# Kernel optimization log

Hardware: AMD Instinct MI355X
Metric: run time of the kernel (lower is better)

The kernel has to match this reference:

```python
import jax, jax.numpy as jnp
import numpy as np

B, S, D_MODEL, N_HEADS, HEAD_DIM = 4, 2048, 1024, 16, 64
NEG = -1e9


def apply_rope_real(x, cos_f, sin_f):
    # x: [B, H, S, D]; cos_f/sin_f: [S, D//2] broadcast over B, H
    x_even = x[..., ::2]
    x_odd = x[..., 1::2]
    out_even = x_even * cos_f - x_odd * sin_f
    out_odd = x_even * sin_f + x_odd * cos_f
    return jnp.stack([out_even, out_odd], axis=-1).reshape(x.shape)


def setup_inputs() -> dict:
    key = jax.random.key(0)
    ks = jax.random.split(key, 8)
    x = jax.random.normal(ks[0], (B, S, D_MODEL), dtype=jnp.float32)
    # RoPE tables: theta_i = 10000^{-2i/d}, angles = pos * theta
    inv_freq = 1.0 / (10000.0 ** (jnp.arange(0, HEAD_DIM, 2, dtype=jnp.float32) / HEAD_DIM))
    angles = jnp.arange(S, dtype=jnp.float32)[:, None] * inv_freq[None, :]  # [S, D/2]
    cos_freqs = jnp.cos(angles)
    sin_freqs = jnp.sin(angles)
    causal_mask = jnp.where(jnp.tril(jnp.ones((S, S), dtype=bool)), 0.0, NEG).astype(jnp.float32)
    scale = 0.02
    w_q = jax.random.normal(ks[1], (D_MODEL, D_MODEL), dtype=jnp.float32) * scale
    w_k = jax.random.normal(ks[2], (D_MODEL, D_MODEL), dtype=jnp.float32) * scale
    w_v = jax.random.normal(ks[3], (D_MODEL, D_MODEL), dtype=jnp.float32) * scale
    w_o = jax.random.normal(ks[4], (D_MODEL, D_MODEL), dtype=jnp.float32) * scale
    return {"x": x, "cos_freqs": cos_freqs, "sin_freqs": sin_freqs,
            "causal_mask": causal_mask, "w_q": w_q, "w_k": w_k, "w_v": w_v, "w_o": w_o}


def reference(x, cos_freqs, sin_freqs, causal_mask, w_q, w_k, w_v, w_o):
    batch, seq_len, _ = x.shape
    scale = 1.0 / jnp.sqrt(jnp.float32(HEAD_DIM))
    # torch Linear: y = x @ W.T
    def proj(w):
        return (x @ w.T).reshape(batch, seq_len, N_HEADS, HEAD_DIM).transpose(0, 2, 1, 3)
    q = apply_rope_real(proj(w_q), cos_freqs, sin_freqs)
    k = apply_rope_real(proj(w_k), cos_freqs, sin_freqs)
    v = proj(w_v)
    attn = jnp.einsum('bhqd,bhkd->bhqk', q, k) * scale + causal_mask
    attn = jax.nn.softmax(attn, axis=-1)
    out = jnp.einsum('bhqk,bhkd->bhqd', attn, v)
    out = out.transpose(0, 2, 1, 3).reshape(batch, seq_len, -1)
    return out @ w_o.T
```

## Files before the change

kernel.cpp:

```cpp
#include <hip/hip_runtime.h>
#include <stdint.h>

#define B_  4
#define S_  2048
#define DM_ 1024
#define NH_ 16
#define HD_ 64

typedef unsigned short ushort_t;
typedef __bf16 bf16x8 __attribute__((ext_vector_type(8)));
typedef float  floatx4 __attribute__((ext_vector_type(4)));
typedef float  floatx16 __attribute__((ext_vector_type(16)));

__device__ __forceinline__ float bf2f(ushort_t u) {
    union { unsigned int i; float f; } v; v.i = ((unsigned int)u) << 16; return v.f;
}
__device__ __forceinline__ ushort_t f2bf(float f) {
    union { float f; unsigned int i; } v; v.f = f;
    unsigned int x = v.i;
    return (ushort_t)((x + 0x7fffu + ((x >> 16) & 1u)) >> 16);
}
__device__ __forceinline__ unsigned int pack_bf16_trunc(float lo, float hi) {
    union { float f; unsigned int u; } a, b;
    a.f = lo; b.f = hi;
    return __builtin_amdgcn_perm(b.u, a.u, 0x07060302u);
}

#define QSCALE 0.1803368801f

__global__ __launch_bounds__(256) void cvt_all_kernel(
    const float* __restrict__ x,  const float* __restrict__ wq,
    const float* __restrict__ wk, const float* __restrict__ wv,
    const float* __restrict__ wo,
    ushort_t* __restrict__ xb,  ushort_t* __restrict__ wqb,
    ushort_t* __restrict__ wkb, ushort_t* __restrict__ wvb,
    ushort_t* __restrict__ wob)
{
    const int blk = blockIdx.x;
    const float* src; ushort_t* dst; int off;
    if (blk < 8192)       { src = x;  dst = xb;  off = blk; }
    else if (blk < 9216)  { src = wq; dst = wqb; off = blk - 8192; }
    else if (blk < 10240) { src = wk; dst = wkb; off = blk - 9216; }
    else if (blk < 11264) { src = wv; dst = wvb; off = blk - 10240; }
    else                  { src = wo; dst = wob; off = blk - 11264; }
    const int i = off * 256 + threadIdx.x;
    float4 v = ((const float4*)src)[i];
    ushort4 o; o.x = f2bf(v.x); o.y = f2bf(v.y); o.z = f2bf(v.z); o.w = f2bf(v.w);
    ((ushort4*)dst)[i] = o;
}

__global__ __launch_bounds__(512, 2) void gemm_qkv_kernel(
    const ushort_t* __restrict__ A,
    const ushort_t* __restrict__ B0, const ushort_t* __restrict__ B1,
    const ushort_t* __restrict__ B2,
    void* __restrict__ C0, void* __restrict__ C1, void* __restrict__ C2,
    const float* __restrict__ cf, const float* __restrict__ sf,
    int M, int N, int K, int nz)
{
    __shared__ ushort_t As[2][16384];
    __shared__ ushort_t Bs[2][8192];

    const int lid = blockIdx.x;
    const int cpx = gridDim.x >> 3;
    const int wg  = (lid & 7) * cpx + (lid >> 3);
    const int x   = wg / (8 * nz);
    const int rr  = wg - x * (8 * nz);
    const int y   = rr & 7;
    const int z   = rr >> 3;

    const ushort_t* Bw = z == 0 ? B0 : z == 1 ? B1 : B2;
    void* Cv           = z == 0 ? C0 : z == 1 ? C1 : C2;

    const int tid  = threadIdx.x;
    const int wave = tid >> 6, lane = tid & 63;
    const int l15 = lane & 15, quad = lane >> 4;
    const int wr = wave >> 1, wc = wave & 1;
    const int mbase = x * 256;
    const int nbase = y * 128;
    const int NT = K >> 6;

    auto stageA = [&](int bt, int t, int L0) {
#pragma unroll
        for (int L = L0; L < L0 + 2; ++L) {
            const int e8  = L * 512 + tid;
            const int row = e8 >> 3, c = e8 & 7;
            const ushort_t* src = A + (size_t)(mbase + row) * K + t * 64 + ((c ^ (row & 7)) << 3);
            __builtin_amdgcn_global_load_lds(
                (const __attribute__((address_space(1))) unsigned int*)src,
                (__attribute__((address_space(3))) unsigned int*)(&As[bt][e8 * 8]), 16, 0, 0);
        }
    };
    auto stageB = [&](int bt, int t, int L) {
        const int e8  = L * 512 + tid;
        const int row = e8 >> 3, c = e8 & 7;
        const ushort_t* src = Bw + (size_t)(nbase + row) * K + t * 64 + ((c ^ (row & 7)) << 3);
        __builtin_amdgcn_global_load_lds(
            (const __attribute__((address_space(1))) unsigned int*)src,
            (__attribute__((address_space(3))) unsigned int*)(&Bs[bt][e8 * 8]), 16, 0, 0);
    };

    floatx4 acc[4][4] = {};

    stageA(0, 0, 0); stageA(0, 0, 2);
    stageB(0, 0, 0); stageB(0, 0, 1);
    if (NT > 1) {
        stageB(1, 1, 0); stageB(1, 1, 1);
        asm volatile("s_waitcnt vmcnt(2)" ::: "memory");
    } else {
        asm volatile("s_waitcnt vmcnt(0)" ::: "memory");
    }
    __builtin_amdgcn_s_barrier();

    auto do_tile = [&](int t, int bt) {
        bf16x8 a0[2][2], a1[2][2], b0[2][2], b1[2][2];
#pragma unroll
        for (int kk = 0; kk < 2; ++kk) {
#pragma unroll
            for (int f = 0; f < 2; ++f) {
                const int row = wr * 64 + f * 16 + l15;
                a0[kk][f] = *(const bf16x8*)&As[bt][row * 64 + ((((kk << 2) | quad)) ^ (l15 & 7)) * 8];
            }
#pragma unroll
            for (int g = 0; g < 2; ++g) {
                const int row = wc * 64 + g * 16 + l15;
                b0[kk][g] = *(const bf16x8*)&Bs[bt][row * 64 + ((((kk << 2) | quad)) ^ (l15 & 7)) * 8];
            }
        }
        if (t + 1 < NT) stageA(bt ^ 1, t + 1, 0);
        __builtin_amdgcn_s_barrier();
        asm volatile("s_waitcnt lgkmcnt(0)" ::: "memory");
        __builtin_amdgcn_s_setprio(1);
#pragma unroll
        for (int kk = 0; kk < 2; ++kk)
#pragma unroll
            for (int mt = 0; mt < 2; ++mt)
#pragma unroll
                for (int nt = 0; nt < 2; ++nt)
                    acc[mt][nt] = __builtin_amdgcn_mfma_f32_16x16x32_bf16(
                        a0[kk][mt], b0[kk][nt], acc[mt][nt], 0, 0, 0);
        __builtin_amdgcn_s_setprio(0);
        __builtin_amdgcn_s_barrier();

#pragma unroll
        for (int kk = 0; kk < 2; ++kk)
#pragma unroll
            for (int g = 0; g < 2; ++g) {
                const int row = wc * 64 + 32 + g * 16 + l15;
                b1[kk][g] = *(const bf16x8*)&Bs[bt][row * 64 + ((((kk << 2) | quad)) ^ (l15 & 7)) * 8];
            }
        if (t + 1 < NT) stageA(bt ^ 1, t + 1, 2);
        __builtin_amdgcn_s_barrier();
        asm volatile("s_waitcnt lgkmcnt(0)" ::: "memory");
        __builtin_amdgcn_s_setprio(1);
#pragma unroll
        for (int kk = 0; kk < 2; ++kk)
#pragma unroll
            for (int mt = 0; mt < 2; ++mt)
#pragma unroll
                for (int nt = 0; nt < 2; ++nt)
                    acc[mt][2 + nt] = __builtin_amdgcn_mfma_f32_16x16x32_bf16(
                        a0[kk][mt], b1[kk][nt], acc[mt][2 + nt], 0, 0, 0);
        __builtin_amdgcn_s_setprio(0);
        __builtin_amdgcn_s_barrier();

#pragma unroll
        for (int kk = 0; kk < 2; ++kk)
#pragma unroll
            for (int f = 0; f < 2; ++f) {
                const int row = wr * 64 + 32 + f * 16 + l15;
                a1[kk][f] = *(const bf16x8*)&As[bt][row * 64 + ((((kk << 2) | quad)) ^ (l15 & 7)) * 8];
            }
        if (t + 2 < NT) stageB(bt, t + 2, 0);
        __builtin_amdgcn_s_barrier();
        asm volatile("s_waitcnt lgkmcnt(0)" ::: "memory");
        __builtin_amdgcn_s_setprio(1);
#pragma unroll
        for (int kk = 0; kk < 2; ++kk)
#pragma unroll
            for (int mt = 0; mt < 2; ++mt)
#pragma unroll
                for (int nt = 0; nt < 2; ++nt)
                    acc[2 + mt][2 + nt] = __builtin_amdgcn_mfma_f32_16x16x32_bf16(
                        a1[kk][mt], b1[kk][nt], acc[2 + mt][2 + nt], 0, 0, 0);
        __builtin_amdgcn_s_setprio(0);
        __builtin_amdgcn_s_barrier();

        if (t + 2 < NT) stageB(bt, t + 2, 1);
        __builtin_amdgcn_s_barrier();
        __builtin_amdgcn_s_setprio(1);
#pragma unroll
        for (int kk = 0; kk < 2; ++kk)
#pragma unroll
            for (int mt = 0; mt < 2; ++mt)
#pragma unroll
                for (int nt = 0; nt < 2; ++nt)
                    acc[2 + mt][nt] = __builtin_amdgcn_mfma_f32_16x16x32_bf16(
                        a1[kk][mt], b0[kk][nt], acc[2 + mt][nt], 0, 0, 0);
        __builtin_amdgcn_s_setprio(0);
        if (t + 2 < NT) { asm volatile("s_waitcnt vmcnt(2)" ::: "memory"); }
        else            { asm volatile("s_waitcnt vmcnt(0)" ::: "memory"); }
        __builtin_amdgcn_s_barrier();
    };

    for (int t = 0; t < NT; t += 2) {
        do_tile(t, 0);
        do_tile(t + 1, 1);
    }

    const float qs = (z == 0) ? QSCALE : 1.0f;
#pragma unroll
    for (int mt = 0; mt < 4; ++mt) {
#pragma unroll
        for (int nt = 0; nt < 4; ++nt) {
            const int col = nbase + wc * 64 + nt * 16 + l15;
            const int m0  = mbase + wr * 64 + mt * 16 + quad * 4;
            if (z == 2) {
                const int b = m0 >> 11, s = m0 & 2047;
                const int hh = col >> 6, d = col & 63;
                uint2 pk;
                pk.x = (unsigned)f2bf(acc[mt][nt][0]) | ((unsigned)f2bf(acc[mt][nt][1]) << 16);
                pk.y = (unsigned)f2bf(acc[mt][nt][2]) | ((unsigned)f2bf(acc[mt][nt][3]) << 16);
                *(uint2*)&((ushort_t*)Cv)[((size_t)((b * NH_ + hh) * HD_ + d)) * S_ + s] = pk;
            } else {
                const int d = col & 63, j = d >> 1;
                const int hh = col >> 6;
                const float sgn = (l15 & 1) ? 1.0f : -1.0f;
#pragma unroll
                for (int r = 0; r < 4; ++r) {
                    const int m = m0 + r;
                    const int b = m >> 11, s = m & 2047;
                    const float v = acc[mt][nt][r];
                    const float p = __shfl_xor(v, 1, 64);
                    const float c  = cf[s * 32 + j] * qs;
                    const float sn = sf[s * 32 + j] * qs * sgn;
                    ((ushort_t*)Cv)[(((size_t)(b * NH_ + hh)) * S_ + s) * HD_ + d] =
                        f2bf(v * c + p * sn);
                }
            }
        }
    }
}

__global__ __launch_bounds__(256, 2) void gemm_proj_kernel(
    const ushort_t* __restrict__ A, const ushort_t* __restrict__ Bw,
    float* __restrict__ Cv, int M, int N, int K)
{
    __shared__ ushort_t As[2][8192];
    __shared__ ushort_t Bs[2][8192];

    const int lid = blockIdx.x;
    const int cpx = gridDim.x >> 3;
    const int wg  = (lid & 7) * cpx + (lid >> 3);
    const int x   = wg >> 3;
    const int y   = wg & 7;

    const int tid  = threadIdx.x;
    const int wave = tid >> 6, lane = tid & 63;
    const int l15 = lane & 15, quad = lane >> 4;
    const int wr = wave >> 1, wc = wave & 1;
    const int mbase = x * 128;
    const int nbase = y * 128;
    const int NT = K >> 6;

    auto stageA = [&](int bt, int t) {
#pragma unroll
        for (int L = 0; L < 4; ++L) {
            const int e   = L * 256 + tid;
            const int row = e >> 3, c = e & 7;
            const ushort_t* src = A + (size_t)(mbase + row) * K + t * 64 + ((c ^ (row & 7)) << 3);
            __builtin_amdgcn_global_load_lds(
                (const __attribute__((address_space(1))) unsigned int*)src,
                (__attribute__((address_space(3))) unsigned int*)(&As[bt][e * 8]), 16, 0, 0);
        }
    };
    auto stageB = [&](int bt, int t) {
#pragma unroll
        for (int L = 0; L < 4; ++L) {
            const int e   = L * 256 + tid;
            const int row = e >> 3, c = e & 7;
            const ushort_t* src = Bw + (size_t)(nbase + row) * K + t * 64 + ((c ^ (row & 7)) << 3);
            __builtin_amdgcn_global_load_lds(
                (const __attribute__((address_space(1))) unsigned int*)src,
                (__attribute__((address_space(3))) unsigned int*)(&Bs[bt][e * 8]), 16, 0, 0);
        }
    };

    floatx4 acc[4][4] = {};

    stageA(0, 0);
    stageB(0, 0);
    if (NT > 1) {
        stageB(1, 1);
        asm volatile("s_waitcnt vmcnt(4)" ::: "memory");
    } else {
        asm volatile("s_waitcnt vmcnt(0)" ::: "memory");
    }
    __builtin_amdgcn_s_barrier();

    for (int t = 0; t < NT; ++t) {
        const int bt = t & 1;
        bf16x8 a0[2][2], a1[2][2], bf[2][4];

#pragma unroll
        for (int kk = 0; kk < 2; ++kk) {
#pragma unroll
            for (int f = 0; f < 2; ++f) {
                const int row = wr * 64 + f * 16 + l15;
                a0[kk][f] = *(const bf16x8*)&As[bt][row * 64 + ((((kk << 2) | quad)) ^ (l15 & 7)) * 8];
            }
#pragma unroll
            for (int g = 0; g < 4; ++g) {
                const int row = wc * 64 + g * 16 + l15;
                bf[kk][g] = *(const bf16x8*)&Bs[bt][row * 64 + ((((kk << 2) | quad)) ^ (l15 & 7)) * 8];
            }
        }
        if (t + 1 < NT) stageA(bt ^ 1, t + 1);
        asm volatile("s_waitcnt lgkmcnt(8)" ::: "memory");
        __builtin_amdgcn_s_barrier();
        asm volatile("s_waitcnt lgkmcnt(0)" ::: "memory");
        __builtin_amdgcn_s_setprio(1);
#pragma unroll
        for (int kk = 0; kk < 2; ++kk)
#pragma unroll
            for (int mt = 0; mt < 2; ++mt)
#pragma unroll
                for (int nt = 0; nt < 4; ++nt)
                    acc[mt][nt] = __builtin_amdgcn_mfma_f32_16x16x32_bf16(
                        a0[kk][mt], bf[kk][nt], acc[mt][nt], 0, 0, 0);
        __builtin_amdgcn_s_setprio(0);
        __builtin_amdgcn_s_barrier();

#pragma unroll
        for (int kk = 0; kk < 2; ++kk)
#pragma unroll
            for (int f = 0; f < 2; ++f) {
                const int row = wr * 64 + 32 + f * 16 + l15;
                a1[kk][f] = *(const bf16x8*)&As[bt][row * 64 + ((((kk << 2) | quad)) ^ (l15 & 7)) * 8];
            }
        if (t + 2 < NT) stageB(bt, t + 2);
        __builtin_amdgcn_s_barrier();
        asm volatile("s_waitcnt lgkmcnt(0)" ::: "memory");
        __builtin_amdgcn_s_setprio(1);
#pragma unroll
        for (int kk = 0; kk < 2; ++kk)
#pragma unroll
            for (int mt = 0; mt < 2; ++mt)
#pragma unroll
                for (int nt = 0; nt < 4; ++nt)
                    acc[2 + mt][nt] = __builtin_amdgcn_mfma_f32_16x16x32_bf16(
                        a1[kk][mt], bf[kk][nt], acc[2 + mt][nt], 0, 0, 0);
        __builtin_amdgcn_s_setprio(0);
        if (t + 2 < NT) { asm volatile("s_waitcnt vmcnt(4)" ::: "memory"); }
        else            { asm volatile("s_waitcnt vmcnt(0)" ::: "memory"); }
        __builtin_amdgcn_s_barrier();
    }

#pragma unroll
    for (int mt = 0; mt < 4; ++mt) {
#pragma unroll
        for (int nt = 0; nt < 4; ++nt) {
            const int col = nbase + wc * 64 + nt * 16 + l15;
            const int m0  = mbase + wr * 64 + mt * 16 + quad * 4;
#pragma unroll
            for (int r = 0; r < 4; ++r)
                Cv[(size_t)(m0 + r) * N + col] = acc[mt][nt][r];
        }
    }
}

__global__ __launch_bounds__(256, 4) void attn_kernel(
    const ushort_t* __restrict__ Qg, const ushort_t* __restrict__ Kg,
    const ushort_t* __restrict__ Vg, ushort_t* __restrict__ Og)
{
    __shared__ ushort_t Ks[2][64 * 64];
    __shared__ ushort_t Vt[2][64 * 64];

    const int id   = blockIdx.x;
    const int sg   = id >> 3;
    const int bh   = (id & 7) * 8 + (sg & 7);
    const int qtile = 15 - (sg >> 3);
    const int tid  = threadIdx.x;
    const int wave = tid >> 6, lane = tid & 63;
    const int l31 = lane & 31, h = lane >> 5;

    const size_t bh_off = (size_t)bh * S_ * HD_;
    const int b_out = bh >> 4, h_out = bh & 15;

    const int e0 = tid, e1 = tid + 256;
    const int r0 = e0 >> 3, c0 = (e0 & 7) ^ (r0 & 7);
    const int r1 = e1 >> 3, c1 = (e1 & 7) ^ (r1 & 7);

    const int qbase = qtile * 128;
    const int nkt   = 2 * qtile + 2;
    const int qrow  = qbase + wave * 32 + l31;

    bf16x8 qf[4];
#pragma unroll
    for (int ks = 0; ks < 4; ++ks)
        qf[ks] = *(const bf16x8*)(Qg + bh_off + (size_t)qrow * HD_ + ks * 16 + h * 8);

    float m_run = -1e30f, l_run = 0.f;
    floatx16 o_acc[2] = {};

    {
        const ushort_t* ka = Kg + bh_off + (size_t)r0 * HD_ + c0 * 8;
        const ushort_t* kb = Kg + bh_off + (size_t)r1 * HD_ + c1 * 8;
        const ushort_t* va = Vg + bh_off + (size_t)r0 * S_ + c0 * 8;
        const ushort_t* vb = Vg + bh_off + (size_t)r1 * S_ + c1 * 8;
        __builtin_amdgcn_global_load_lds(
            (const __attribute__((address_space(1))) unsigned int*)ka,
            (__attribute__((address_space(3))) unsigned int*)(&Ks[0][e0 * 8]), 16, 0, 0);
        __builtin_amdgcn_global_load_lds(
            (const __attribute__((address_space(1))) unsigned int*)kb,
            (__attribute__((address_space(3))) unsigned int*)(&Ks[0][e1 * 8]), 16, 0, 0);
        __builtin_amdgcn_global_load_lds(
            (const __attribute__((address_space(1))) unsigned int*)va,
            (__attribute__((address_space(3))) unsigned int*)(&Vt[0][e0 * 8]), 16, 0, 0);
        __builtin_amdgcn_global_load_lds(
            (const __attribute__((address_space(1))) unsigned int*)vb,
            (__attribute__((address_space(3))) unsigned int*)(&Vt[0][e1 * 8]), 16, 0, 0);
    }
    asm volatile("s_waitcnt vmcnt(0)" ::: "memory");
    __syncthreads();

    for (int kt = 0; kt < nkt; ++kt) {
        const int kbase = kt * 64;
        const int cur = kt & 1;

        if (kt + 1 < nkt) {
            const int nb = kbase + 64;
            const ushort_t* ka = Kg + bh_off + (size_t)(nb + r0) * HD_ + c0 * 8;
            const ushort_t* kb = Kg + bh_off + (size_t)(nb + r1) * HD_ + c1 * 8;
            const ushort_t* va = Vg + bh_off + (size_t)r0 * S_ + nb + c0 * 8;
            const ushort_t* vb = Vg + bh_off + (size_t)r1 * S_ + nb + c1 * 8;
            __builtin_amdgcn_global_load_lds(
                (const __attribute__((address_space(1))) unsigned int*)ka,
                (__attribute__((address_space(3))) unsigned int*)(&Ks[cur ^ 1][e0 * 8]), 16, 0, 0);
            __builtin_amdgcn_global_load_lds(
                (const __attribute__((address_space(1))) unsigned int*)kb,
                (__attribute__((address_space(3))) unsigned int*)(&Ks[cur ^ 1][e1 * 8]), 16, 0, 0);
            __builtin_amdgcn_global_load_lds(
                (const __attribute__((address_space(1))) unsigned int*)va,
                (__attribute__((address_space(3))) unsigned int*)(&Vt[cur ^ 1][e0 * 8]), 16, 0, 0);
            __builtin_amdgcn_global_load_lds(
                (const __attribute__((address_space(1))) unsigned int*)vb,
                (__attribute__((address_space(3))) unsigned int*)(&Vt[cur ^ 1][e1 * 8]), 16, 0, 0);
        }

        if (kbase <= qbase + wave * 32 + 31) {
            floatx16 st[2] = {};
#pragma unroll
            for (int nt = 0; nt < 2; ++nt) {
                const int krow = nt * 32 + l31;
#pragma unroll
                for (int ks = 0; ks < 4; ++ks) {
                    bf16x8 kf = *(const bf16x8*)&Ks[cur][krow * 64 +
                                    (((ks * 2 + h) ^ (l31 & 7)) << 3)];
                    st[nt] = __builtin_amdgcn_mfma_f32_32x32x16_bf16(kf, qf[ks], st[nt], 0, 0, 0);
                }
            }
            if (kbase + 63 > qbase + wave * 32) {
#pragma unroll
                for (int nt = 0; nt < 2; ++nt) {
                    const int key0 = kbase + nt * 32 + 4 * h;
#pragma unroll
                    for (int c = 0; c < 4; ++c)
#pragma unroll
                        for (int r = 0; r < 4; ++r)
                            if (key0 + 8 * c + r > qrow) st[nt][c * 4 + r] = -1e9f;
                }
            }
            float mx = st[0][0];
#pragma unroll
            for (int nt = 0; nt < 2; ++nt)
#pragma unroll
                for (int i = 0; i < 16; ++i) mx = fmaxf(mx, st[nt][i]);
            mx = fmaxf(mx, __shfl_xor(mx, 32, 64));
            if (!__all(mx <= m_run + 8.0f)) {
                const float mnew = fmaxf(m_run, mx);
                const float alpha = __builtin_amdgcn_exp2f(m_run - mnew);
                m_run = mnew;
                l_run *= alpha;
#pragma unroll
                for (int dt = 0; dt < 2; ++dt)
#pragma unroll
                    for (int i = 0; i < 16; ++i) o_acc[dt][i] *= alpha;
            }
            float sum = 0.f;
#pragma unroll
            for (int nt = 0; nt < 2; ++nt)
#pragma unroll
                for (int i = 0; i < 16; ++i) {
                    const float p = __builtin_amdgcn_exp2f(st[nt][i] - m_run);
                    st[nt][i] = p; sum += p;
                }
            sum += __shfl_xor(sum, 32, 64);
            l_run += sum;

            bf16x8 pf[4];
#pragma unroll
            for (int ks = 0; ks < 4; ++ks) {
                const int nt = ks >> 1, base = (ks & 1) * 8;
                unsigned wrd[4];
#pragma unroll
                for (int d8 = 0; d8 < 2; ++d8) {
                    unsigned p = pack_bf16_trunc(st[nt][base + 2 * d8],
                                                 st[nt][base + 2 * d8 + 1]);
                    unsigned q = pack_bf16_trunc(st[nt][base + 4 + 2 * d8],
                                                 st[nt][base + 4 + 2 * d8 + 1]);
                    auto r = __builtin_amdgcn_permlane32_swap((int)p, (int)q, false, false);
                    wrd[d8]     = (unsigned)r[0];
                    wrd[2 + d8] = (unsigned)r[1];
                }
                union { unsigned u[4]; bf16x8 v; } cvt;
                cvt.u[0] = wrd[0]; cvt.u[1] = wrd[1];
                cvt.u[2] = wrd[2]; cvt.u[3] = wrd[3];
                pf[ks] = cvt.v;
            }

#pragma unroll
            for (int dt = 0; dt < 2; ++dt) {
                const int d = dt * 32 + l31;
#pragma unroll
                for (int ks = 0; ks < 4; ++ks) {
                    bf16x8 vf = *(const bf16x8*)&Vt[cur][d * 64 +
                                    (((ks * 2 + h) ^ (l31 & 7)) << 3)];
                    o_acc[dt] = __builtin_amdgcn_mfma_f32_32x32x16_bf16(vf, pf[ks], o_acc[dt], 0, 0, 0);
                }
            }
        }

        asm volatile("s_waitcnt vmcnt(0)" ::: "memory");
        __syncthreads();
    }

    const float inv = 1.0f / l_run;
    ushort_t* orow = Og + ((size_t)(b_out * S_ + qrow)) * DM_ + h_out * HD_;
#pragma unroll
    for (int dt = 0; dt < 2; ++dt)
#pragma unroll
        for (int c = 0; c < 4; ++c) {
            uint2 pk;
            pk.x = (unsigned)f2bf(o_acc[dt][c * 4 + 0] * inv) |
                   ((unsigned)f2bf(o_acc[dt][c * 4 + 1] * inv) << 16);
            pk.y = (unsigned)f2bf(o_acc[dt][c * 4 + 2] * inv) |
                   ((unsigned)f2bf(o_acc[dt][c * 4 + 3] * inv) << 16);
            *(uint2*)(orow + dt * 32 + 8 * c + 4 * h) = pk;
        }
}

extern "C" void kernel_launch(void* const* d_in, const int* in_sizes, int n_in,
                              void* d_out, int out_size, void* d_ws, size_t ws_size,
                              hipStream_t stream)
{
    const float* x  = (const float*)d_in[0];
    const float* cf = (const float*)d_in[1];
    const float* sf = (const float*)d_in[2];
    const float* wq = (const float*)d_in[4];
    const float* wk = (const float*)d_in[5];
    const float* wv = (const float*)d_in[6];
    const float* wo = (const float*)d_in[7];
    float* out = (float*)d_out;

    const size_t NELEM = (size_t)B_ * S_ * DM_;
    const size_t WELEM = (size_t)DM_ * DM_;
    ushort_t* xb  = (ushort_t*)d_ws;
    ushort_t* qb  = xb + NELEM;
    ushort_t* kb  = qb + NELEM;
    ushort_t* vb  = kb + NELEM;
    ushort_t* ao  = vb + NELEM;
    ushort_t* wqb = ao + NELEM;
    ushort_t* wkb = wqb + WELEM;
    ushort_t* wvb = wkb + WELEM;
    ushort_t* wob = wvb + WELEM;

    cvt_all_kernel<<<dim3(8192 + 4 * 1024), 256, 0, stream>>>(
        x, wq, wk, wv, wo, xb, wqb, wkb, wvb, wob);

    const int M = B_ * S_;
    gemm_qkv_kernel<<<dim3(32 * 8 * 3), 512, 0, stream>>>(
        xb, wqb, wkb, wvb, qb, kb, vb, cf, sf, M, DM_, DM_, 3);
    attn_kernel<<<dim3(1024), 256, 0, stream>>>(qb, kb, vb, ao);
    gemm_proj_kernel<<<dim3(64 * 8), 256, 0, stream>>>(
        ao, wob, out, M, DM_, DM_);
}
```

Before: 259.3 us.

## Use 4-wave QKV GEMM with larger per-wave tiles; interleave attention q-tile order

The QKV GEMM drops from 8 waves to 4 waves per block on the same 256x128 tile. Each wave now computes a 128x64 sub-tile with 32 accumulators, and the K loop becomes one tile per iteration with two MFMA phases instead of four. This raises register reuse per LDS read and cuts barriers, at the cost of more VGPR pressure and fewer waves to hide latency. Separately, the attention kernel reorders q-tiles with a table that interleaves long and short causal tiles, aiming at better load balance across CUs.

```diff
diff --git a/kernel.cpp b/kernel.cpp
--- a/kernel.cpp
+++ b/kernel.cpp
@@ -49,7 +49,7 @@
     ((ushort4*)dst)[i] = o;
 }
 
-__global__ __launch_bounds__(512, 2) void gemm_qkv_kernel(
+__global__ __launch_bounds__(256, 1) void gemm_qkv_kernel(
     const ushort_t* __restrict__ A,
     const ushort_t* __restrict__ B0, const ushort_t* __restrict__ B1,
     const ushort_t* __restrict__ B2,
@@ -79,10 +79,10 @@
     const int nbase = y * 128;
     const int NT = K >> 6;
 
-    auto stageA = [&](int bt, int t, int L0) {
-#pragma unroll
-        for (int L = L0; L < L0 + 2; ++L) {
-            const int e8  = L * 512 + tid;
+    auto stageA = [&](int bt, int t) {
+#pragma unroll
+        for (int L = 0; L < 8; ++L) {
+            const int e8  = L * 256 + tid;
             const int row = e8 >> 3, c = e8 & 7;
             const ushort_t* src = A + (size_t)(mbase + row) * K + t * 64 + ((c ^ (row & 7)) << 3);
             __builtin_amdgcn_global_load_lds(
@@ -90,130 +90,94 @@
                 (__attribute__((address_space(3))) unsigned int*)(&As[bt][e8 * 8]), 16, 0, 0);
         }
     };
-    auto stageB = [&](int bt, int t, int L) {
-        const int e8  = L * 512 + tid;
-        const int row = e8 >> 3, c = e8 & 7;
-        const ushort_t* src = Bw + (size_t)(nbase + row) * K + t * 64 + ((c ^ (row & 7)) << 3);
-        __builtin_amdgcn_global_load_lds(
-            (const __attribute__((address_space(1))) unsigned int*)src,
-            (__attribute__((address_space(3))) unsigned int*)(&Bs[bt][e8 * 8]), 16, 0, 0);
+    auto stageB = [&](int bt, int t) {
+#pragma unroll
+        for (int L = 0; L < 4; ++L) {
+            const int e8  = L * 256 + tid;
+            const int row = e8 >> 3, c = e8 & 7;
+            const ushort_t* src = Bw + (size_t)(nbase + row) * K + t * 64 + ((c ^ (row & 7)) << 3);
+            __builtin_amdgcn_global_load_lds(
+                (const __attribute__((address_space(1))) unsigned int*)src,
+                (__attribute__((address_space(3))) unsigned int*)(&Bs[bt][e8 * 8]), 16, 0, 0);
+        }
     };
 
-    floatx4 acc[4][4] = {};
-
-    stageA(0, 0, 0); stageA(0, 0, 2);
-    stageB(0, 0, 0); stageB(0, 0, 1);
+    floatx4 acc[8][4] = {};
+
+    stageA(0, 0);
+    stageB(0, 0);
     if (NT > 1) {
-        stageB(1, 1, 0); stageB(1, 1, 1);
-        asm volatile("s_waitcnt vmcnt(2)" ::: "memory");
+        stageB(1, 1);
+        asm volatile("s_waitcnt vmcnt(4)" ::: "memory");
     } else {
         asm volatile("s_waitcnt vmcnt(0)" ::: "memory");
     }
     __builtin_amdgcn_s_barrier();
 
-    auto do_tile = [&](int t, int bt) {
-        bf16x8 a0[2][2], a1[2][2], b0[2][2], b1[2][2];
+    for (int t = 0; t < NT; ++t) {
+        const int bt = t & 1;
+        bf16x8 a0[2][4], a1[2][4], bf[2][4];
+
 #pragma unroll
         for (int kk = 0; kk < 2; ++kk) {
 #pragma unroll
-            for (int f = 0; f < 2; ++f) {
-                const int row = wr * 64 + f * 16 + l15;
+            for (int f = 0; f < 4; ++f) {
+                const int row = wr * 128 + f * 16 + l15;
                 a0[kk][f] = *(const bf16x8*)&As[bt][row * 64 + ((((kk << 2) | quad)) ^ (l15 & 7)) * 8];
             }
 #pragma unroll
-            for (int g = 0; g < 2; ++g) {
+            for (int g = 0; g < 4; ++g) {
                 const int row = wc * 64 + g * 16 + l15;
-                b0[kk][g] = *(const bf16x8*)&Bs[bt][row * 64 + ((((kk << 2) | quad)) ^ (l15 & 7)) * 8];
-            }
-        }
-        if (t + 1 < NT) stageA(bt ^ 1, t + 1, 0);
+                bf[kk][g] = *(const bf16x8*)&Bs[bt][row * 64 + ((((kk << 2) | quad)) ^ (l15 & 7)) * 8];
+            }
+        }
+        if (t + 1 < NT) stageA(bt ^ 1, t + 1);
         __builtin_amdgcn_s_barrier();
         asm volatile("s_waitcnt lgkmcnt(0)" ::: "memory");
         __builtin_amdgcn_s_setprio(1);
 #pragma unroll
         for (int kk = 0; kk < 2; ++kk)
 #pragma unroll
-            for (int mt = 0; mt < 2; ++mt)
-#pragma unroll
-                for (int nt = 0; nt < 2; ++nt)
+            for (int mt = 0; mt < 4; ++mt)
+#pragma unroll
+                for (int nt = 0; nt < 4; ++nt)
                     acc[mt][nt] = __builtin_amdgcn_mfma_f32_16x16x32_bf16(
-                        a0[kk][mt], b0[kk][nt], acc[mt][nt], 0, 0, 0);
+                        a0[kk][mt], bf[kk][nt], acc[mt][nt], 0, 0, 0);
         __builtin_amdgcn_s_setprio(0);
         __builtin_amdgcn_s_barrier();
 
 #pragma unroll
         for (int kk = 0; kk < 2; ++kk)
 #pragma unroll
-            for (int g = 0; g < 2; ++g) {
-                const int row = wc * 64 + 32 + g * 16 + l15;
-                b1[kk][g] = *(const bf16x8*)&Bs[bt][row * 64 + ((((kk << 2) | quad)) ^ (l15 & 7)) * 8];
-            }
-        if (t + 1 < NT) stageA(bt ^ 1, t + 1, 2);
+            for (int f = 0; f < 4; ++f) {
+                const int row = wr * 128 + 64 + f * 16 + l15;
+                a1[kk][f] = *(const bf16x8*)&As[bt][row * 64 + ((((kk << 2) | quad)) ^ (l15 & 7)) * 8];
+            }
+        if (t + 2 < NT) stageB(bt, t + 2);
         __builtin_amdgcn_s_barrier();
         asm volatile("s_waitcnt lgkmcnt(0)" ::: "memory");
         __builtin_amdgcn_s_setprio(1);
 #pragma unroll
         for (int kk = 0; kk < 2; ++kk)
 #pragma unroll
-            for (int mt = 0; mt < 2; ++mt)
-#pragma unroll
-                for (int nt = 0; nt < 2; ++nt)
-                    acc[mt][2 + nt] = __builtin_amdgcn_mfma_f32_16x16x32_bf16(
-                        a0[kk][mt], b1[kk][nt], acc[mt][2 + nt], 0, 0, 0);
+            for (int mt = 0; mt < 4; ++mt)
+#pragma unroll
+                for (int nt = 0; nt < 4; ++nt)
+                    acc[4 + mt][nt] = __builtin_amdgcn_mfma_f32_16x16x32_bf16(
+                        a1[kk][mt], bf[kk][nt], acc[4 + mt][nt], 0, 0, 0);
         __builtin_amdgcn_s_setprio(0);
-        __builtin_amdgcn_s_barrier();
-
-#pragma unroll
-        for (int kk = 0; kk < 2; ++kk)
-#pragma unroll
-            for (int f = 0; f < 2; ++f) {
-                const int row = wr * 64 + 32 + f * 16 + l15;
-                a1[kk][f] = *(const bf16x8*)&As[bt][row * 64 + ((((kk << 2) | quad)) ^ (l15 & 7)) * 8];
-            }
-        if (t + 2 < NT) stageB(bt, t + 2, 0);
-        __builtin_amdgcn_s_barrier();
-        asm volatile("s_waitcnt lgkmcnt(0)" ::: "memory");
-        __builtin_amdgcn_s_setprio(1);
-#pragma unroll
-        for (int kk = 0; kk < 2; ++kk)
-#pragma unroll
-            for (int mt = 0; mt < 2; ++mt)
-#pragma unroll
-                for (int nt = 0; nt < 2; ++nt)
-                    acc[2 + mt][2 + nt] = __builtin_amdgcn_mfma_f32_16x16x32_bf16(
-                        a1[kk][mt], b1[kk][nt], acc[2 + mt][2 + nt], 0, 0, 0);
-        __builtin_amdgcn_s_setprio(0);
-        __builtin_amdgcn_s_barrier();
-
-        if (t + 2 < NT) stageB(bt, t + 2, 1);
-        __builtin_amdgcn_s_barrier();
-        __builtin_amdgcn_s_setprio(1);
-#pragma unroll
-        for (int kk = 0; kk < 2; ++kk)
-#pragma unroll
-            for (int mt = 0; mt < 2; ++mt)
-#pragma unroll
-                for (int nt = 0; nt < 2; ++nt)
-                    acc[2 + mt][nt] = __builtin_amdgcn_mfma_f32_16x16x32_bf16(
-                        a1[kk][mt], b0[kk][nt], acc[2 + mt][nt], 0, 0, 0);
-        __builtin_amdgcn_s_setprio(0);
-        if (t + 2 < NT) { asm volatile("s_waitcnt vmcnt(2)" ::: "memory"); }
+        if (t + 2 < NT) { asm volatile("s_waitcnt vmcnt(4)" ::: "memory"); }
         else            { asm volatile("s_waitcnt vmcnt(0)" ::: "memory"); }
         __builtin_amdgcn_s_barrier();
-    };
-
-    for (int t = 0; t < NT; t += 2) {
-        do_tile(t, 0);
-        do_tile(t + 1, 1);
     }
 
     const float qs = (z == 0) ? QSCALE : 1.0f;
 #pragma unroll
-    for (int mt = 0; mt < 4; ++mt) {
+    for (int mt = 0; mt < 8; ++mt) {
 #pragma unroll
         for (int nt = 0; nt < 4; ++nt) {
             const int col = nbase + wc * 64 + nt * 16 + l15;
-            const int m0  = mbase + wr * 64 + mt * 16 + quad * 4;
+            const int m0  = mbase + wr * 128 + mt * 16 + quad * 4;
             if (z == 2) {
                 const int b = m0 >> 11, s = m0 & 2047;
                 const int hh = col >> 6, d = col & 63;
@@ -375,10 +339,12 @@
     __shared__ ushort_t Ks[2][64 * 64];
     __shared__ ushort_t Vt[2][64 * 64];
 
+    const int qt_tab[16] = {15,13,11,9, 0,2,4,6, 14,12,10,8, 1,3,5,7};
+
     const int id   = blockIdx.x;
     const int sg   = id >> 3;
     const int bh   = (id & 7) * 8 + (sg & 7);
-    const int qtile = 15 - (sg >> 3);
+    const int qtile = qt_tab[sg >> 3];
     const int tid  = threadIdx.x;
     const int wave = tid >> 6, lane = tid & 63;
     const int l31 = lane & 31, h = lane >> 5;
@@ -578,7 +544,7 @@
         x, wq, wk, wv, wo, xb, wqb, wkb, wvb, wob);
 
     const int M = B_ * S_;
-    gemm_qkv_kernel<<<dim3(32 * 8 * 3), 512, 0, stream>>>(
+    gemm_qkv_kernel<<<dim3(32 * 8 * 3), 256, 0, stream>>>(
         xb, wqb, wkb, wvb, qb, kb, vb, cf, sf, M, DM_, DM_, 3);
     attn_kernel<<<dim3(1024), 256, 0, stream>>>(qb, kb, vb, ao);
     gemm_proj_kernel<<<dim3(64 * 8), 256, 0, stream>>>(
```

Result: slower. 274.8 us (+6.0%).
